# Kernel tuning notes

Hardware: AMD Instinct MI355X
Metric: run time of the kernel (lower is better)

## Reference

```python
import jax, jax.numpy as jnp
import numpy as np

DIM = 256
NUM_HEADS = 8
HEAD_DIM = DIM // NUM_HEADS


def setup_inputs() -> dict:
    key = jax.random.key(0)
    k_x, k_wq, k_bq, k_wp, k_bp = jax.random.split(key, 5)
    x = jax.random.normal(k_x, (4, DIM, 64, 64), dtype=jnp.float32)
    # 1x1 convs == per-pixel linear layers over channels
    w_qkv = jax.random.normal(k_wq, (3 * DIM, DIM), dtype=jnp.float32) * (DIM ** -0.5)
    b_qkv = jax.random.normal(k_bq, (3 * DIM,), dtype=jnp.float32) * 0.02
    w_proj = jax.random.normal(k_wp, (DIM, DIM), dtype=jnp.float32) * (DIM ** -0.5)
    b_proj = jax.random.normal(k_bp, (DIM,), dtype=jnp.float32) * 0.02
    return {"x": x, "w_qkv": w_qkv, "b_qkv": b_qkv, "w_proj": w_proj, "b_proj": b_proj}


def reference(x, w_qkv, b_qkv, w_proj, b_proj):
    B, C, H, W = x.shape
    S = H * W
    h, d = NUM_HEADS, HEAD_DIM
    # flatten spatial dims: (B, C, H, W) -> (B, S, C)
    xf = x.reshape(B, C, S).transpose(0, 2, 1)
    # 1x1 conv qkv: (B, S, 3C)
    qkv = xf @ w_qkv.T + b_qkv
    q, k, v = jnp.split(qkv, 3, axis=-1)
    # channel dim splits as (heads, head_dim): (B, S, C) -> (B, h, S, d)
    split = lambda t: t.reshape(B, S, h, d).transpose(0, 2, 1, 3)
    q, k, v = split(q), split(k), split(v)
    scale = d ** -0.5
    attn = jnp.einsum('bhsd,bhtd->bhst', q, k) * scale  # (B, h, S, S)
    attn = jax.nn.softmax(attn, axis=-1)
    out = jnp.einsum('bhst,bhtd->bhsd', attn, v)
    # merge heads: (B, h, S, d) -> (B, S, C)
    out = out.transpose(0, 2, 1, 3).reshape(B, S, C)
    out = out @ w_proj.T + b_proj
    # back to (B, C, H, W)
    return out.transpose(0, 2, 1).reshape(B, C, H, W)
```

## Files before the change

kernel.cpp:

```cpp
#include <hip/hip_runtime.h>


typedef __attribute__((ext_vector_type(8))) short short8;
typedef __attribute__((ext_vector_type(4))) float f4;

__device__ __forceinline__ short f2bs(float f) {
  union { float f; unsigned u; } v; v.f = f;
  unsigned r = v.u + 0x7FFFu + ((v.u >> 16) & 1u);
  return (short)(r >> 16);
}

__device__ __forceinline__ short8 cvt8(f4 a, f4 b) {
  short8 o;
  o[0] = f2bs(a[0]); o[1] = f2bs(a[1]); o[2] = f2bs(a[2]); o[3] = f2bs(a[3]);
  o[4] = f2bs(b[0]); o[5] = f2bs(b[1]); o[6] = f2bs(b[2]); o[7] = f2bs(b[3]);
  return o;
}

__global__ __launch_bounds__(256) void k_qkv(
    const float* __restrict__ x, const float* __restrict__ w,
    const float* __restrict__ bias,
    short* __restrict__ Qt, short* __restrict__ Kq, short* __restrict__ Vt) {
  const int tid = threadIdx.x;
  const int L = tid & 63, wv = tid >> 6;
  const int ln15 = L & 15, quad = L >> 4;
  const int mt = blockIdx.x;
  const int b = mt >> 6;
  const int s0 = (mt & 63) << 6;
  const int j0 = blockIdx.y << 6;
  const int jw = j0 + wv * 16;

  f4 acc[4] = {{0,0,0,0},{0,0,0,0},{0,0,0,0},{0,0,0,0}};
  const float* wb = w + (jw + ln15) * 256 + quad * 8;
  const float* xb = x + b * (256 * 4096) + s0 + ln15;

#pragma unroll 2
  for (int cb = 0; cb < 256; cb += 32) {
    f4 a0 = *(const f4*)(wb + cb);
    f4 a1 = *(const f4*)(wb + cb + 4);
    short8 af = cvt8(a0, a1);
    const float* xc = xb + (cb + quad * 8) * 4096;
#pragma unroll
    for (int sub = 0; sub < 4; ++sub) {
      const float* xs = xc + sub * 16;
      short8 bf;
#pragma unroll
      for (int jj = 0; jj < 8; ++jj) bf[jj] = f2bs(xs[jj * 4096]);
      acc[sub] = __builtin_amdgcn_mfma_f32_16x16x32_bf16(af, bf, acc[sub], 0, 0, 0);
    }
  }

  float bj[4];
#pragma unroll
  for (int r = 0; r < 4; ++r) bj[r] = bias[jw + quad * 4 + r];

  const int type = j0 >> 8;
  if (type == 0) {
    const float qs = 0.17677669529663689f * 1.44269504088896f;
    const int h = jw >> 5;
    const int dbase = jw & 31;
#pragma unroll
    for (int r = 0; r < 4; ++r) {
      const int d = dbase + quad * 4 + r;
      short* qp = Qt + (size_t)((b * 8 + h) * 32 + d) * 4096 + s0 + ln15;
#pragma unroll
      for (int sub = 0; sub < 4; ++sub)
        qp[sub * 16] = f2bs((acc[sub][r] + bj[r]) * qs);
    }
  } else if (type == 2) {
    const int jv = jw - 512;
    const int h = jv >> 5;
    const int dbase = jv & 31;
#pragma unroll
    for (int r = 0; r < 4; ++r) {
      const int d = dbase + quad * 4 + r;
      short* vp = Vt + (size_t)((b * 8 + h) * 32 + d) * 4096 + s0 + ln15;
#pragma unroll
      for (int sub = 0; sub < 4; ++sub)
        vp[sub * 16] = f2bs(acc[sub][r] + bj[r]);
    }
  } else {
    __shared__ __align__(16) short tl[4 * 64 * 16];
    short* tw = tl + wv * 1024;
#pragma unroll
    for (int sub = 0; sub < 4; ++sub) {
      const int s = sub * 16 + ln15;
      const int swz = (s >> 2) & 1;
#pragma unroll
      for (int r = 0; r < 4; ++r) {
        const int dl = quad * 4 + r;
        tw[s * 16 + (((dl >> 3) ^ swz) * 8) + (dl & 7)] = f2bs(acc[sub][r] + bj[r]);
      }
    }
    const int h = (jw - 256) >> 5;
    const int d0 = (jw - 256) & 31;
#pragma unroll
    for (int i = 0; i < 2; ++i) {
      const int sl = i * 32 + (L >> 1);
      const int gg = L & 1;
      const int g2 = gg ^ ((sl >> 2) & 1);
      short8 row = *(const short8*)(tw + sl * 16 + g2 * 8);
      *(short8*)(Kq + (size_t)((b * 8 + h) * 4096 + s0 + sl) * 32 + d0 + gg * 8) = row;
    }
  }
}

__global__ __launch_bounds__(256) void k_attn(
    const short* __restrict__ Qt, const short* __restrict__ Kq,
    const short* __restrict__ Vt, short* __restrict__ O) {
  const int tid = threadIdx.x;
  const int L = tid & 63, wv = tid >> 6;
  const int ln15 = L & 15, quad = L >> 4;
  const int bh = blockIdx.y;
  const int b = bh >> 3, h = bh & 7;
  const int qb = blockIdx.x * 128 + wv * 32;

  const short* Qb = Qt + (size_t)bh * 32 * 4096;
  const short* Kb = Kq + (size_t)bh * 4096 * 32;
  const short* Vb = Vt + (size_t)bh * 32 * 4096;

  __shared__ __align__(16) short plds[4 * 2048];
  short* pw = plds + wv * 2048;

  short8 qf[2];
#pragma unroll
  for (int qs = 0; qs < 2; ++qs)
#pragma unroll
    for (int jj = 0; jj < 8; ++jj)
      qf[qs][jj] = Qb[(quad * 8 + jj) * 4096 + qb + qs * 16 + ln15];

  f4 acc[2][2] = {{{0,0,0,0},{0,0,0,0}},{{0,0,0,0},{0,0,0,0}}};
  float lsum[2][4] = {{0,0,0,0},{0,0,0,0}};

  const int hb = ln15 >> 3, ln7 = ln15 & 7;
  const int swzr = ln15 >> 1;
  const short* kp = Kb + ln15 * 32 + quad * 8;
  const short* vp0 = Vb + ln15 * 4096 + quad * 8;
  const short* vp1 = vp0 + 16 * 4096;

#pragma unroll 2
  for (int kb = 0; kb < 4096; kb += 64) {
#pragma unroll
    for (int t = 0; t < 4; ++t) {
      short8 kf = *(const short8*)(kp + (kb + t * 16) * 32);
#pragma unroll
      for (int qs = 0; qs < 2; ++qs) {
        f4 z = {0.f, 0.f, 0.f, 0.f};
        f4 sc = __builtin_amdgcn_mfma_f32_16x16x32_bf16(qf[qs], kf, z, 0, 0, 0);
#pragma unroll
        for (int r = 0; r < 4; ++r) {
          float p = __builtin_amdgcn_exp2f(sc[r]);
          lsum[qs][r] += p;
          const int gp = (t * 2 + hb) ^ (quad * 2 + (r >> 1));
          pw[(qs * 16 + quad * 4 + r) * 64 + gp * 8 + ln7] = f2bs(p);
        }
      }
    }
#pragma unroll
    for (int kk = 0; kk < 2; ++kk) {
      short8 vf0 = *(const short8*)(vp0 + kb + kk * 32);
      short8 vf1 = *(const short8*)(vp1 + kb + kk * 32);
#pragma unroll
      for (int qs = 0; qs < 2; ++qs) {
        const int gp = (kk * 4 + quad) ^ swzr;
        short8 pf = *(const short8*)(pw + (qs * 16 + ln15) * 64 + gp * 8);
        acc[qs][0] = __builtin_amdgcn_mfma_f32_16x16x32_bf16(pf, vf0, acc[qs][0], 0, 0, 0);
        acc[qs][1] = __builtin_amdgcn_mfma_f32_16x16x32_bf16(pf, vf1, acc[qs][1], 0, 0, 0);
      }
    }
  }

#pragma unroll
  for (int qs = 0; qs < 2; ++qs)
#pragma unroll
    for (int r = 0; r < 4; ++r) {
      float l = lsum[qs][r];
      l += __shfl_xor(l, 1);
      l += __shfl_xor(l, 2);
      l += __shfl_xor(l, 4);
      l += __shfl_xor(l, 8);
      const float rl = 1.0f / l;
      const int sg = qb + qs * 16 + quad * 4 + r;
      short* op = O + (size_t)(b * 4096 + sg) * 256 + h * 32 + ln15;
      op[0]  = f2bs(acc[qs][0][r] * rl);
      op[16] = f2bs(acc[qs][1][r] * rl);
    }
}

__global__ __launch_bounds__(256) void k_proj(
    const short* __restrict__ O, const float* __restrict__ w,
    const float* __restrict__ bias, float* __restrict__ out) {
  const int tid = threadIdx.x;
  const int L = tid & 63, wv = tid >> 6;
  const int ln15 = L & 15, quad = L >> 4;
  const int m0 = blockIdx.x * 64 + wv * 16;
  const int n0 = blockIdx.y << 6;
  const int b = m0 >> 12, s0 = m0 & 4095;

  f4 acc[4] = {{0,0,0,0},{0,0,0,0},{0,0,0,0},{0,0,0,0}};
  const short* Ob = O + (size_t)(m0 + ln15) * 256 + quad * 8;
  const float* wb = w + (n0 + ln15) * 256 + quad * 8;

#pragma unroll 2
  for (int cb = 0; cb < 256; cb += 32) {
    short8 af = *(const short8*)(Ob + cb);
#pragma unroll
    for (int sub = 0; sub < 4; ++sub) {
      f4 b0 = *(const f4*)(wb + sub * (16 * 256) + cb);
      f4 b1 = *(const f4*)(wb + sub * (16 * 256) + cb + 4);
      short8 bf = cvt8(b0, b1);
      acc[sub] = __builtin_amdgcn_mfma_f32_16x16x32_bf16(af, bf, acc[sub], 0, 0, 0);
    }
  }

  __shared__ float tl[4][64 * 17];
  float* tw = tl[wv];
#pragma unroll
  for (int sub = 0; sub < 4; ++sub) {
    const float bv = bias[n0 + sub * 16 + ln15];
#pragma unroll
    for (int r = 0; r < 4; ++r)
      tw[(sub * 16 + ln15) * 17 + quad * 4 + r] = acc[sub][r] + bv;
  }
#pragma unroll
  for (int i = 0; i < 4; ++i) {
    const int c = i * 16 + (L >> 2);
    const int ms = (L & 3) * 4;
    f4 v;
#pragma unroll
    for (int j = 0; j < 4; ++j) v[j] = tw[c * 17 + ms + j];
    *(f4*)(out + (size_t)b * (256 * 4096) + (size_t)(n0 + c) * 4096 + s0 + ms) = v;
  }
}

extern "C" void kernel_launch(void* const* d_in, const int* in_sizes, int n_in,
                              void* d_out, int out_size, void* d_ws, size_t ws_size,
                              hipStream_t stream) {
  const float* x      = (const float*)d_in[0];
  const float* w_qkv  = (const float*)d_in[1];
  const float* b_qkv  = (const float*)d_in[2];
  const float* w_proj = (const float*)d_in[3];
  const float* b_proj = (const float*)d_in[4];
  float* out = (float*)d_out;

  const size_t SEG = (size_t)4 * 8 * 4096 * 32;
  short* Qt = (short*)d_ws;
  short* Kq = Qt + SEG;
  short* Vt = Kq + SEG;
  short* O  = Vt + SEG;

  k_qkv <<<dim3(256, 12), 256, 0, stream>>>(x, w_qkv, b_qkv, Qt, Kq, Vt);
  k_attn<<<dim3(32, 32),  256, 0, stream>>>(Qt, Kq, Vt, O);
  k_proj<<<dim3(256, 4),  256, 0, stream>>>(O, w_proj, b_proj, out);
}
```

Baseline: 348.5 us.

## Swap QK MFMA operands so P stores pack into wide LDS writes

Q is now stored row-major (s, d) like K, using the same LDS-transpose path in the QKV kernel, so the attention kernel loads Q fragments with one vector load. The score MFMA is computed as K·Q instead of Q·K, so each lane holds four consecutive key columns for one query. That lets the exp'd probabilities be packed with a bf16 pair-convert and written to LDS as 8-byte stores instead of scalar short stores. The row-sum reduction also shrinks to two cross-quad shuffles plus a broadcast. The aim is to cut LDS store instructions and conversion ALU in the inner softmax loop, at the cost of a new swizzle pattern whose bank-conflict behaviour is unverified.

```diff
diff --git a/kernel.cpp b/kernel.cpp
--- a/kernel.cpp
+++ b/kernel.cpp
@@ -17,10 +17,23 @@
   return o;
 }
 
+#if __has_builtin(__builtin_amdgcn_cvt_pk_bf16_f32)
+__device__ __forceinline__ int pk2(float a, float b) {
+  auto v = __builtin_amdgcn_cvt_pk_bf16_f32(a, b);
+  int r;
+  __builtin_memcpy(&r, &v, 4);
+  return r;
+}
+#else
+__device__ __forceinline__ int pk2(float a, float b) {
+  return (int)((unsigned short)f2bs(a) | ((unsigned)f2bs(b) << 16));
+}
+#endif
+
 __global__ __launch_bounds__(256) void k_qkv(
     const float* __restrict__ x, const float* __restrict__ w,
     const float* __restrict__ bias,
-    short* __restrict__ Qt, short* __restrict__ Kq, short* __restrict__ Vt) {
+    short* __restrict__ Qr, short* __restrict__ Kq, short* __restrict__ Vt) {
   const int tid = threadIdx.x;
   const int L = tid & 63, wv = tid >> 6;
   const int ln15 = L & 15, quad = L >> 4;
@@ -30,6 +43,8 @@
   const int j0 = blockIdx.y << 6;
   const int jw = j0 + wv * 16;
 
+  __shared__ __align__(16) short tl[4 * 64 * 16];
+
   f4 acc[4] = {{0,0,0,0},{0,0,0,0},{0,0,0,0},{0,0,0,0}};
   const float* wb = w + (jw + ln15) * 256 + quad * 8;
   const float* xb = x + b * (256 * 4096) + s0 + ln15;
@@ -55,19 +70,7 @@
   for (int r = 0; r < 4; ++r) bj[r] = bias[jw + quad * 4 + r];
 
   const int type = j0 >> 8;
-  if (type == 0) {
-    const float qs = 0.17677669529663689f * 1.44269504088896f;
-    const int h = jw >> 5;
-    const int dbase = jw & 31;
-#pragma unroll
-    for (int r = 0; r < 4; ++r) {
-      const int d = dbase + quad * 4 + r;
-      short* qp = Qt + (size_t)((b * 8 + h) * 32 + d) * 4096 + s0 + ln15;
-#pragma unroll
-      for (int sub = 0; sub < 4; ++sub)
-        qp[sub * 16] = f2bs((acc[sub][r] + bj[r]) * qs);
-    }
-  } else if (type == 2) {
+  if (type == 2) {
     const int jv = jw - 512;
     const int h = jv >> 5;
     const int dbase = jv & 31;
@@ -80,7 +83,10 @@
         vp[sub * 16] = f2bs(acc[sub][r] + bj[r]);
     }
   } else {
-    __shared__ __align__(16) short tl[4 * 64 * 16];
+    const float qsc = 0.17677669529663689f * 1.44269504088896f;
+    const float mul = (type == 0) ? qsc : 1.0f;
+    short* dst = (type == 0) ? Qr : Kq;
+    const int hj = jw & 255;
     short* tw = tl + wv * 1024;
 #pragma unroll
     for (int sub = 0; sub < 4; ++sub) {
@@ -89,24 +95,24 @@
 #pragma unroll
       for (int r = 0; r < 4; ++r) {
         const int dl = quad * 4 + r;
-        tw[s * 16 + (((dl >> 3) ^ swz) * 8) + (dl & 7)] = f2bs(acc[sub][r] + bj[r]);
-      }
-    }
-    const int h = (jw - 256) >> 5;
-    const int d0 = (jw - 256) & 31;
+        tw[s * 16 + (((dl >> 3) ^ swz) * 8) + (dl & 7)] = f2bs((acc[sub][r] + bj[r]) * mul);
+      }
+    }
+    const int h = hj >> 5;
+    const int d0 = hj & 31;
 #pragma unroll
     for (int i = 0; i < 2; ++i) {
       const int sl = i * 32 + (L >> 1);
       const int gg = L & 1;
       const int g2 = gg ^ ((sl >> 2) & 1);
       short8 row = *(const short8*)(tw + sl * 16 + g2 * 8);
-      *(short8*)(Kq + (size_t)((b * 8 + h) * 4096 + s0 + sl) * 32 + d0 + gg * 8) = row;
+      *(short8*)(dst + (size_t)((b * 8 + h) * 4096 + s0 + sl) * 32 + d0 + gg * 8) = row;
     }
   }
 }
 
 __global__ __launch_bounds__(256) void k_attn(
-    const short* __restrict__ Qt, const short* __restrict__ Kq,
+    const short* __restrict__ Qr, const short* __restrict__ Kq,
     const short* __restrict__ Vt, short* __restrict__ O) {
   const int tid = threadIdx.x;
   const int L = tid & 63, wv = tid >> 6;
@@ -115,28 +121,24 @@
   const int b = bh >> 3, h = bh & 7;
   const int qb = blockIdx.x * 128 + wv * 32;
 
-  const short* Qb = Qt + (size_t)bh * 32 * 4096;
+  const short* Qb = Qr + (size_t)bh * 4096 * 32;
   const short* Kb = Kq + (size_t)bh * 4096 * 32;
   const short* Vb = Vt + (size_t)bh * 32 * 4096;
 
   __shared__ __align__(16) short plds[4 * 2048];
   short* pw = plds + wv * 2048;
+  const int swz = (ln15 & 7) << 1;
 
   short8 qf[2];
 #pragma unroll
   for (int qs = 0; qs < 2; ++qs)
-#pragma unroll
-    for (int jj = 0; jj < 8; ++jj)
-      qf[qs][jj] = Qb[(quad * 8 + jj) * 4096 + qb + qs * 16 + ln15];
+    qf[qs] = *(const short8*)(Qb + (qb + qs * 16 + ln15) * 32 + quad * 8);
 
   f4 acc[2][2] = {{{0,0,0,0},{0,0,0,0}},{{0,0,0,0},{0,0,0,0}}};
-  float lsum[2][4] = {{0,0,0,0},{0,0,0,0}};
-
-  const int hb = ln15 >> 3, ln7 = ln15 & 7;
-  const int swzr = ln15 >> 1;
+  float lsum[2] = {0.f, 0.f};
+
   const short* kp = Kb + ln15 * 32 + quad * 8;
-  const short* vp0 = Vb + ln15 * 4096 + quad * 8;
-  const short* vp1 = vp0 + 16 * 4096;
+  const short* vp = Vb + ln15 * 4096 + quad * 8;
 
 #pragma unroll 2
   for (int kb = 0; kb < 4096; kb += 64) {
@@ -146,45 +148,51 @@
 #pragma unroll
       for (int qs = 0; qs < 2; ++qs) {
         f4 z = {0.f, 0.f, 0.f, 0.f};
-        f4 sc = __builtin_amdgcn_mfma_f32_16x16x32_bf16(qf[qs], kf, z, 0, 0, 0);
-#pragma unroll
-        for (int r = 0; r < 4; ++r) {
-          float p = __builtin_amdgcn_exp2f(sc[r]);
-          lsum[qs][r] += p;
-          const int gp = (t * 2 + hb) ^ (quad * 2 + (r >> 1));
-          pw[(qs * 16 + quad * 4 + r) * 64 + gp * 8 + ln7] = f2bs(p);
-        }
-      }
-    }
-#pragma unroll
-    for (int kk = 0; kk < 2; ++kk) {
-      short8 vf0 = *(const short8*)(vp0 + kb + kk * 32);
-      short8 vf1 = *(const short8*)(vp1 + kb + kk * 32);
+        f4 sc = __builtin_amdgcn_mfma_f32_16x16x32_bf16(kf, qf[qs], z, 0, 0, 0);
+        float p0 = __builtin_amdgcn_exp2f(sc[0]);
+        float p1 = __builtin_amdgcn_exp2f(sc[1]);
+        float p2 = __builtin_amdgcn_exp2f(sc[2]);
+        float p3 = __builtin_amdgcn_exp2f(sc[3]);
+        lsum[qs] += (p0 + p1) + (p2 + p3);
+        int2 pr;
+        pr.x = pk2(p0, p1);
+        pr.y = pk2(p2, p3);
+        const int g = (4 * t + quad) ^ swz;
+        *(int2*)(pw + qs * 1024 + ln15 * 64 + g * 4) = pr;
+      }
+    }
+#pragma unroll
+    for (int ks = 0; ks < 2; ++ks) {
+      short8 pf[2];
 #pragma unroll
       for (int qs = 0; qs < 2; ++qs) {
-        const int gp = (kk * 4 + quad) ^ swzr;
-        short8 pf = *(const short8*)(pw + (qs * 16 + ln15) * 64 + gp * 8);
-        acc[qs][0] = __builtin_amdgcn_mfma_f32_16x16x32_bf16(pf, vf0, acc[qs][0], 0, 0, 0);
-        acc[qs][1] = __builtin_amdgcn_mfma_f32_16x16x32_bf16(pf, vf1, acc[qs][1], 0, 0, 0);
-      }
-    }
-  }
-
-#pragma unroll
-  for (int qs = 0; qs < 2; ++qs)
+        const int g0 = (8 * ks + 2 * quad) ^ swz;
+        pf[qs] = *(const short8*)(pw + qs * 1024 + ln15 * 64 + g0 * 4);
+      }
+#pragma unroll
+      for (int dg = 0; dg < 2; ++dg) {
+        short8 vf = *(const short8*)(vp + dg * (16 * 4096) + kb + ks * 32);
+        acc[0][dg] = __builtin_amdgcn_mfma_f32_16x16x32_bf16(pf[0], vf, acc[0][dg], 0, 0, 0);
+        acc[1][dg] = __builtin_amdgcn_mfma_f32_16x16x32_bf16(pf[1], vf, acc[1][dg], 0, 0, 0);
+      }
+    }
+  }
+
+#pragma unroll
+  for (int qs = 0; qs < 2; ++qs) {
+    float l = lsum[qs];
+    l += __shfl_xor(l, 16);
+    l += __shfl_xor(l, 32);
+    const float rl = 1.0f / l;
 #pragma unroll
     for (int r = 0; r < 4; ++r) {
-      float l = lsum[qs][r];
-      l += __shfl_xor(l, 1);
-      l += __shfl_xor(l, 2);
-      l += __shfl_xor(l, 4);
-      l += __shfl_xor(l, 8);
-      const float rl = 1.0f / l;
+      const float rlr = __shfl(rl, quad * 4 + r);
       const int sg = qb + qs * 16 + quad * 4 + r;
       short* op = O + (size_t)(b * 4096 + sg) * 256 + h * 32 + ln15;
-      op[0]  = f2bs(acc[qs][0][r] * rl);
-      op[16] = f2bs(acc[qs][1][r] * rl);
-    }
+      op[0]  = f2bs(acc[qs][0][r] * rlr);
+      op[16] = f2bs(acc[qs][1][r] * rlr);
+    }
+  }
 }
 
 __global__ __launch_bounds__(256) void k_proj(
@@ -244,12 +252,12 @@
   float* out = (float*)d_out;
 
   const size_t SEG = (size_t)4 * 8 * 4096 * 32;
-  short* Qt = (short*)d_ws;
-  short* Kq = Qt + SEG;
+  short* Qr = (short*)d_ws;
+  short* Kq = Qr + SEG;
   short* Vt = Kq + SEG;
   short* O  = Vt + SEG;
 
-  k_qkv <<<dim3(256, 12), 256, 0, stream>>>(x, w_qkv, b_qkv, Qt, Kq, Vt);
-  k_attn<<<dim3(32, 32),  256, 0, stream>>>(Qt, Kq, Vt, O);
+  k_qkv <<<dim3(256, 12), 256, 0, stream>>>(x, w_qkv, b_qkv, Qr, Kq, Vt);
+  k_attn<<<dim3(32, 32),  256, 0, stream>>>(Qr, Kq, Vt, O);
   k_proj<<<dim3(256, 4),  256, 0, stream>>>(O, w_proj, b_proj, out);
 }
```

New measurement: 352.8 us. No clear change (+1.2%).
